# Kernel optimization log

Hardware: AMD Instinct MI355X
Metric: run time of the kernel (lower is better)

The kernel has to match this reference:

```python
import jax, jax.numpy as jnp
import numpy as np

C = 64
K = 3          # kernel_size
EK = 5         # encoder_kernel
PAD = (K - 1) // 2


def _conv(x, w, pad):
    return jax.lax.conv_general_dilated(
        x, w, window_strides=(1, 1), padding=[(pad, pad), (pad, pad)],
        dimension_numbers=('NCHW', 'OIHW', 'NCHW'))


def setup_inputs() -> dict:
    key = jax.random.key(0)
    ks = jax.random.split(key, 6)
    b, h, w = 8, 128, 128
    x = jax.random.normal(ks[0], (b, C, h, w), dtype=jnp.float32)
    # gen_kernel: 1x1 conv (C->C, with bias) then EKxEK conv (C->K*K, no bias)
    w1 = jax.random.normal(ks[1], (C, C, 1, 1), dtype=jnp.float32) * (1.0 / np.sqrt(C))
    b1 = jax.random.normal(ks[2], (C,), dtype=jnp.float32) * 0.01
    w2 = jax.random.normal(ks[3], (K * K, C, EK, EK), dtype=jnp.float32) * (1.0 / np.sqrt(C * EK * EK))
    # consensus t_c: 1x1 conv C->C//4, relu, 1x1 conv C//4->C, relu (no bias)
    tc1 = jax.random.normal(ks[4], (C // 4, C, 1, 1), dtype=jnp.float32) * (1.0 / np.sqrt(C))
    tc2 = jax.random.normal(ks[5], (C, C // 4, 1, 1), dtype=jnp.float32) * (1.0 / np.sqrt(C // 4))
    return {"x": x, "w1": w1, "b1": b1, "w2": w2, "tc1": tc1, "tc2": tc2}


def reference(x, w1, b1, w2, tc1, tc2):
    b, c, h, w = x.shape
    oh, ow = h, w  # stride == 1
    # dynamic kernel logits: (b, K*K, oh, ow)
    y = _conv(x, w1, 0) + b1[None, :, None, None]
    wt = _conv(y, w2, (EK - 1) // 2)
    # consensus scale: adaptive avg pool to 1x1 then mean over batch -> (c,)
    x_con = jnp.mean(x, axis=(0, 2, 3))                      # (c,)
    h1 = jax.nn.relu(jnp.einsum('oc,c->o', tc1[:, :, 0, 0], x_con))
    tmp = jax.nn.relu(jnp.einsum('oc,c->o', tc2[:, :, 0, 0], h1))  # (c,)
    # broadcast logits to (b, c, K*K, oh, ow) and softmax over K*K
    logits = wt[:, None, :, :, :] * tmp[None, :, None, None, None]
    attn = jax.nn.softmax(logits, axis=2)                    # (b,c,9,oh,ow)
    # unfold patches: reflect-pad then 9 shifted views, order kh*K+kw (row-major)
    px = jnp.pad(x, ((0, 0), (0, 0), (PAD, PAD), (PAD, PAD)), mode='reflect')
    pats = jnp.stack([px[:, :, i:i + oh, j:j + ow]
                      for i in range(K) for j in range(K)], axis=2)  # (b,c,9,oh,ow)
    out = jnp.sum(attn * pats, axis=2)                       # (b,c,oh,ow)
    return out
```

## Files before the change

### kernel.cpp

```cpp
#include <hip/hip_runtime.h>
#include <hip/hip_bf16.h>
#include <cstddef>


#define B 8
#define C 64
#define HW 128
#define NK 9
#define NT 25
#define LOG2E 1.4426950408889634f
#define PSTR 72

typedef __attribute__((ext_vector_type(8))) short short8;
typedef __attribute__((ext_vector_type(4))) float float4v;
typedef __attribute__((ext_vector_type(4))) unsigned int uint4v;

__device__ __forceinline__ unsigned short f2bf(float f) {
    unsigned int u = __float_as_uint(f);
    unsigned int r = u + 0x7FFF + ((u >> 16) & 1);
    return (unsigned short)(r >> 16);
}
__device__ __forceinline__ float fast_exp2(float x) {
    float r;
    asm("v_exp_f32 %0, %1" : "=v"(r) : "v"(x));
    return r;
}
__device__ __forceinline__ float fast_rcp(float x) {
    float r;
    asm("v_rcp_f32 %0, %1" : "=v"(r) : "v"(x));
    return r;
}

__global__ __launch_bounds__(256) void xcon_kernel(const float* __restrict__ x,
                                                   float* __restrict__ part) {
    const int c = blockIdx.x >> 2, qb = blockIdx.x & 3;
    float s = 0.f;
    for (int bb = 0; bb < 2; ++bb) {
        const int b = qb * 2 + bb;
        const float4* p = (const float4*)(x + ((size_t)(b * C + c)) * (HW * HW));
        for (int idx = threadIdx.x; idx < (HW * HW) / 4; idx += 256) {
            float4 v = p[idx];
            s += (v.x + v.y) + (v.z + v.w);
        }
    }
    __shared__ float red[256];
    red[threadIdx.x] = s;
    __syncthreads();
    for (int off = 128; off > 0; off >>= 1) {
        if (threadIdx.x < off) red[threadIdx.x] += red[threadIdx.x + off];
        __syncthreads();
    }
    if (threadIdx.x == 0) part[c * 4 + qb] = red[0];
}

__global__ __launch_bounds__(256) void prep_kernel(const float* __restrict__ w1,
                                                   const float* __restrict__ b1,
                                                   const float* __restrict__ w2,
                                                   unsigned short* __restrict__ Abuf,
                                                   float* __restrict__ betaG) {
    if (blockIdx.x < 50) {
        __shared__ float sw2[NK * 64];
        __shared__ float sw1[64 * 32];
        const int chunk = blockIdx.x;
        const int t = chunk >> 1, ch = chunk & 1;
        for (int idx = threadIdx.x; idx < NK * 64; idx += 256) {
            const int m = idx >> 6, cc = idx & 63;
            sw2[idx] = w2[(m * 64 + cc) * NT + t];
        }
        for (int idx = threadIdx.x; idx < 2048; idx += 256) {
            const int cc = idx >> 5, j = idx & 31;
            sw1[idx] = w1[cc * 64 + ch * 32 + j];
        }
        __syncthreads();
        for (int sidx = 0; sidx < 2; ++sidx) {
            const int slot = sidx * 256 + threadIdx.x;
            const int quad = slot >> 7, m = (slot >> 3) & 15, jj = slot & 7;
            unsigned short hi = 0, lo = 0;
            if (m < NK) {
                float s = 0.f;
                for (int cc = 0; cc < 64; ++cc)
                    s += sw2[m * 64 + cc] * sw1[cc * 32 + quad * 8 + jj];
                hi = f2bf(s);
                lo = f2bf(s - __uint_as_float(((unsigned int)hi) << 16));
            }
            Abuf[chunk * 1024 + slot] = hi;
            Abuf[chunk * 1024 + 512 + slot] = lo;
        }
    } else {
        __shared__ float beta_s[NT * NK];
        const int t0 = threadIdx.x;
        if (t0 < NT * NK) {
            const int t = t0 / NK, k = t0 - t * NK;
            float s = 0.f;
            for (int cc = 0; cc < 64; ++cc)
                s += w2[(k * 64 + cc) * NT + t] * b1[cc];
            beta_s[t0] = s;
        }
        __syncthreads();
        if (t0 < 225) {
            const int ic = t0 / 45, jc = (t0 / 9) % 5, k = t0 % 9;
            float s = 0.f;
            for (int eh = 0; eh < 5; ++eh) {
                bool rok = (ic == 0) ? (eh >= 2) : (ic == 1) ? (eh >= 1)
                          : (ic == 3) ? (eh <= 3) : (ic == 4) ? (eh <= 2) : true;
                if (!rok) continue;
                for (int ew = 0; ew < 5; ++ew) {
                    bool cok = (jc == 0) ? (ew >= 2) : (jc == 1) ? (ew >= 1)
                              : (jc == 3) ? (ew <= 3) : (jc == 4) ? (ew <= 2) : true;
                    if (cok) s += beta_s[(eh * 5 + ew) * NK + k];
                }
            }
            betaG[t0] = s;
        }
    }
}

__global__ __launch_bounds__(512, 4) void fused_kernel(const float* __restrict__ x,
                                                       const unsigned short* __restrict__ Abuf,
                                                       const float* __restrict__ betaG,
                                                       const float* __restrict__ part,
                                                       const float* __restrict__ tc1,
                                                       const float* __restrict__ tc2,
                                                       float* __restrict__ out) {
    __shared__ unsigned short stag[400 * PSTR];
    __shared__ float wpart[128 * 10];
    __shared__ float lt[C];
    const int b = blockIdx.y;
    const int i0 = (blockIdx.x >> 3) * 16, j0 = (blockIdx.x & 7) * 16;
    const int tid = threadIdx.x, lane = tid & 63, wid = tid >> 6;
    const int n = lane & 15, q = lane >> 4;
    const int rowg = wid >> 1, h = wid & 1;

    for (int idx = tid; idx < 12800; idx += 512) {
        const int ch = idx / 200;
        const int rem = idx - ch * 200;
        const int li = rem / 10, cp = rem - li * 10;
        const int gi = i0 + li - 2;
        const int gj = j0 + cp * 2 - 2;
        unsigned int pack = 0u;
        if (gi >= 0 && gi < HW && gj >= 0 && gj <= HW - 2) {
            const float2 v = *(const float2*)(x + (((size_t)(b * C + ch)) * HW + gi) * HW + gj);
            pack = (unsigned int)f2bf(v.x) | ((unsigned int)f2bf(v.y) << 16);
        }
        const int p0 = (li * 20 + cp * 2) * PSTR + ch;
        stag[p0] = (unsigned short)(pack & 0xffffu);
        stag[p0 + PSTR] = (unsigned short)(pack >> 16);
    }

    if (wid == 0) {
        float xcv = (part[lane * 4 + 0] + part[lane * 4 + 1]
                   + part[lane * 4 + 2] + part[lane * 4 + 3]) * (1.f / (B * HW * HW));
        float hh = 0.f;
        for (int c = 0; c < C; ++c) {
            float xcc = __shfl(xcv, c);
            if (lane < 16) hh += tc1[lane * C + c] * xcc;
        }
        hh = fmaxf(hh, 0.f);
        float ltv = 0.f;
#pragma unroll
        for (int o = 0; o < 16; ++o) {
            float ho = __shfl(hh, o);
            ltv += tc2[lane * 16 + o] * ho;
        }
        lt[lane] = fmaxf(ltv, 0.f) * LOG2E;
    }

    const int prow = rowg * 4 + q;
    const int pgi = i0 + prow, pgj = j0 + n;
    float bgv[NK];
    if (h == 0) {
        const int ic = pgi < 2 ? pgi : (pgi > 125 ? pgi - 123 : 2);
        const int jc = pgj < 2 ? pgj : (pgj > 125 ? pgj - 123 : 2);
        const float* bp = betaG + (ic * 5 + jc) * NK;
#pragma unroll
        for (int k = 0; k < NK; ++k) bgv[k] = bp[k];
    }

    __syncthreads();

    float4v acc[4];
    const float4v zero4 = {0.f, 0.f, 0.f, 0.f};
#pragma unroll
    for (int g = 0; g < 4; ++g) acc[g] = zero4;

    const unsigned short* Ab = Abuf + h * 1024 + lane * 8;
    const unsigned short* sb = stag + h * 32 + q * 8;
#pragma unroll
    for (int ew = 0; ew < 5; ++ew) {
        short8 w8[8];
#pragma unroll
        for (int rr = 0; rr < 8; ++rr)
            w8[rr] = *(const short8*)(sb + ((rowg * 4 + rr) * 20 + ew + n) * PSTR);
#pragma unroll
        for (int eh = 0; eh < 5; ++eh) {
            const int t = eh * 5 + ew;
            const short8 ahi = *(const short8*)(Ab + t * 2048);
            const short8 alo = *(const short8*)(Ab + t * 2048 + 512);
#pragma unroll
            for (int g = 0; g < 4; ++g) {
                acc[g] = __builtin_amdgcn_mfma_f32_16x16x32_bf16(ahi, w8[g + eh], acc[g], 0, 0, 0);
                acc[g] = __builtin_amdgcn_mfma_f32_16x16x32_bf16(alo, w8[g + eh], acc[g], 0, 0, 0);
            }
        }
    }

    float wv[NK];
#pragma unroll
    for (int k = 0; k < NK; ++k) {
        const int src = (k >> 2) * 16 + n;
        const int rr = k & 3;
        float v0 = __shfl(acc[0][rr], src);
        float v1 = __shfl(acc[1][rr], src);
        float v2 = __shfl(acc[2][rr], src);
        float v3 = __shfl(acc[3][rr], src);
        wv[k] = (q == 0) ? v0 : (q == 1) ? v1 : (q == 2) ? v2 : v3;
    }

    const int lp = ((rowg & 1) << 6) + lane;
    for (int pg = 0; pg < 2; ++pg) {
        const bool inpass = (rowg >> 1) == pg;
        if (pg) __syncthreads();
        if (inpass && h == 1) {
#pragma unroll
            for (int k = 0; k < NK; ++k) wpart[lp * 10 + k] = wv[k];
        }
        __syncthreads();
        if (inpass && h == 0) {
            float w9[NK];
            float wmax = -1e30f;
#pragma unroll
            for (int k = 0; k < NK; ++k) {
                w9[k] = wv[k] + wpart[lp * 10 + k] + bgv[k];
                wmax = fmaxf(wmax, w9[k]);
            }
#pragma unroll
            for (int k = 0; k < NK; ++k) wpart[lp * 10 + k] = w9[k] - wmax;
        }
        __syncthreads();
#pragma unroll
        for (int s = 0; s < 2; ++s) {
            const int task = tid * 2 + s;
            const int lpx = task >> 3, oct = task & 7;
            const int l6 = lpx & 63;
            const int brow = (2 * pg + (lpx >> 6)) * 4 + (l6 >> 4);
            const int bcol = l6 & 15;
            const int bgi = i0 + brow, bgj = j0 + bcol;
            float dv[NK];
#pragma unroll
            for (int k = 0; k < NK; ++k) dv[k] = wpart[lpx * 10 + k];
            int r0 = bgi - 1; r0 = r0 < 0 ? 1 : r0;
            int r2 = bgi + 1; r2 = r2 > 127 ? 126 : r2;
            int c0 = bgj - 1; c0 = c0 < 0 ? 1 : c0;
            int c2 = bgj + 1; c2 = c2 > 127 ? 126 : c2;
            const int R[3] = {r0 - i0 + 2, bgi - i0 + 2, r2 - i0 + 2};
            const int Cc[3] = {c0 - j0 + 2, bgj - j0 + 2, c2 - j0 + 2};
            const unsigned short* sb2 = stag + oct * 8;
            uint4v xs[NK];
#pragma unroll
            for (int kh = 0; kh < 3; ++kh)
#pragma unroll
                for (int kw = 0; kw < 3; ++kw)
                    xs[kh * 3 + kw] = *(const uint4v*)(sb2 + (R[kh] * 20 + Cc[kw]) * PSTR);
            float* outp = out + (((size_t)b * C + oct * 8) * HW + bgi) * HW + bgj;
#pragma unroll
            for (int jj = 0; jj < 4; ++jj) {
                const float t0 = lt[oct * 8 + jj * 2];
                const float t1 = lt[oct * 8 + jj * 2 + 1];
                float s0 = 0.f, o0 = 0.f, s1 = 0.f, o1 = 0.f;
#pragma unroll
                for (int k = 0; k < NK; ++k) {
                    const unsigned int u = xs[k][jj];
                    const float e0 = fast_exp2(dv[k] * t0);
                    const float e1 = fast_exp2(dv[k] * t1);
                    s0 += e0; o0 = fmaf(e0, __uint_as_float(u << 16), o0);
                    s1 += e1; o1 = fmaf(e1, __uint_as_float(u & 0xffff0000u), o1);
                }
                outp[(size_t)(jj * 2) * (HW * HW)] = o0 * fast_rcp(s0);
                outp[(size_t)(jj * 2 + 1) * (HW * HW)] = o1 * fast_rcp(s1);
            }
        }
    }
}

extern "C" void kernel_launch(void* const* d_in, const int* in_sizes, int n_in,
                              void* d_out, int out_size, void* d_ws, size_t ws_size,
                              hipStream_t stream) {
    const float* x   = (const float*)d_in[0];
    const float* w1  = (const float*)d_in[1];
    const float* b1  = (const float*)d_in[2];
    const float* w2  = (const float*)d_in[3];
    const float* tc1 = (const float*)d_in[4];
    const float* tc2 = (const float*)d_in[5];
    float* out = (float*)d_out;

    char* ws = (char*)d_ws;
    float* part  = (float*)(ws + 0);
    unsigned short* Abuf = (unsigned short*)(ws + 1024);
    float* betaG = (float*)(ws + 103424);

    xcon_kernel<<<256, 256, 0, stream>>>(x, part);
    prep_kernel<<<51, 256, 0, stream>>>(w1, b1, w2, Abuf, betaG);
    fused_kernel<<<dim3(64, B), 512, 0, stream>>>(x, Abuf, betaG, part, tc1, tc2, out);
}
```

Measured before the change: 147.6 us.

## Pre-pack x to padded bf16 channel-last layout and stage tiles via global_load_lds

Adds a separate kernel that converts x once into a zero-padded bf16 NHWC-like buffer whose 64-channel vectors are XOR-swizzled. The fused kernel then fills its shared-memory halo tile with direct 16-byte global-to-LDS loads instead of per-element fp32 loads, conversion and scattered 2-byte LDS stores. LDS reads use the matching XOR swizzle in place of the padded stride, to avoid bank conflicts. The trade-off is an extra kernel launch plus a full write and re-read of a bf16 copy of x through global memory.

New measurement: 146.6 us. No clear change (-0.7%).

```diff
diff --git a/kernel.cpp b/kernel.cpp
--- a/kernel.cpp
+++ b/kernel.cpp
@@ -8,8 +8,8 @@
 #define HW 128
 #define NK 9
 #define NT 25
+#define XR 132
 #define LOG2E 1.4426950408889634f
-#define PSTR 72
 
 typedef __attribute__((ext_vector_type(8))) short short8;
 typedef __attribute__((ext_vector_type(4))) float float4v;
@@ -29,6 +29,12 @@
     float r;
     asm("v_rcp_f32 %0, %1" : "=v"(r) : "v"(x));
     return r;
+}
+__device__ __forceinline__ void load_lds16(const unsigned short* g, unsigned short* l) {
+    __builtin_amdgcn_global_load_lds(
+        (const __attribute__((address_space(1))) unsigned int*)g,
+        (__attribute__((address_space(3))) unsigned int*)l,
+        16, 0, 0);
 }
 
 __global__ __launch_bounds__(256) void xcon_kernel(const float* __restrict__ x,
@@ -51,6 +57,43 @@
         __syncthreads();
     }
     if (threadIdx.x == 0) part[c * 4 + qb] = red[0];
+}
+
+__global__ __launch_bounds__(256) void xpack_kernel(const float* __restrict__ x,
+                                                    unsigned short* __restrict__ xbf) {
+    const int r = blockIdx.x, b = blockIdx.y;
+    unsigned short* rowp = xbf + ((size_t)(b * XR + r)) * (XR * 64);
+    const int t = threadIdx.x;
+    if (r < 2 || r >= 130) {
+        const uint4v z = {0u, 0u, 0u, 0u};
+        for (int idx = t; idx < 1056; idx += 256)
+            *(uint4v*)(rowp + idx * 8) = z;
+        return;
+    }
+    const int h = r - 2;
+    if (t < 32) {
+        const uint4v z = {0u, 0u, 0u, 0u};
+        const int q4 = t & 3;
+        const int wc = (q4 < 2) ? q4 : (q4 + 128);
+        *(uint4v*)(rowp + wc * 64 + ((t >> 2) << 3)) = z;
+    }
+    const int c8 = t >> 5;
+    const int wl = t & 31;
+    const float* xp = x + (((size_t)(b * C + c8 * 8)) * HW + h) * HW;
+#pragma unroll
+    for (int k = 0; k < 4; ++k) {
+        const int gw = wl + 32 * k;
+        const int wc = gw + 2;
+        uint4v dv;
+#pragma unroll
+        for (int j = 0; j < 4; ++j) {
+            const float v0 = xp[(size_t)(2 * j) * (HW * HW) + gw];
+            const float v1 = xp[(size_t)(2 * j + 1) * (HW * HW) + gw];
+            dv[j] = (unsigned int)f2bf(v0) | ((unsigned int)f2bf(v1) << 16);
+        }
+        const int sw = ((r & 1) * 4 + wc) & 7;
+        *(uint4v*)(rowp + wc * 64 + ((c8 ^ sw) << 3)) = dv;
+    }
 }
 
 __global__ __launch_bounds__(256) void prep_kernel(const float* __restrict__ w1,
@@ -115,14 +158,14 @@
     }
 }
 
-__global__ __launch_bounds__(512, 4) void fused_kernel(const float* __restrict__ x,
+__global__ __launch_bounds__(512, 4) void fused_kernel(const unsigned short* __restrict__ xbf,
                                                        const unsigned short* __restrict__ Abuf,
                                                        const float* __restrict__ betaG,
                                                        const float* __restrict__ part,
                                                        const float* __restrict__ tc1,
                                                        const float* __restrict__ tc2,
                                                        float* __restrict__ out) {
-    __shared__ unsigned short stag[400 * PSTR];
+    __shared__ __align__(16) unsigned short stag[400 * 64];
     __shared__ float wpart[128 * 10];
     __shared__ float lt[C];
     const int b = blockIdx.y;
@@ -131,20 +174,21 @@
     const int n = lane & 15, q = lane >> 4;
     const int rowg = wid >> 1, h = wid & 1;
 
-    for (int idx = tid; idx < 12800; idx += 512) {
-        const int ch = idx / 200;
-        const int rem = idx - ch * 200;
-        const int li = rem / 10, cp = rem - li * 10;
-        const int gi = i0 + li - 2;
-        const int gj = j0 + cp * 2 - 2;
-        unsigned int pack = 0u;
-        if (gi >= 0 && gi < HW && gj >= 0 && gj <= HW - 2) {
-            const float2 v = *(const float2*)(x + (((size_t)(b * C + ch)) * HW + gi) * HW + gj);
-            pack = (unsigned int)f2bf(v.x) | ((unsigned int)f2bf(v.y) << 16);
-        }
-        const int p0 = (li * 20 + cp * 2) * PSTR + ch;
-        stag[p0] = (unsigned short)(pack & 0xffffu);
-        stag[p0 + PSTR] = (unsigned short)(pack >> 16);
+    {
+        const unsigned short* xrow0 = xbf + (((size_t)(b * XR + i0)) * XR + j0) * 64;
+#pragma unroll
+        for (int k = 0; k < 6; ++k) {
+            const int ci = k * 512 + tid;
+            const int li = ((ci >> 5) * 205) >> 10;
+            const int rem = ci - li * 160;
+            load_lds16(xrow0 + li * (XR * 64) + rem * 8, stag + ci * 8);
+        }
+        if (tid < 128) {
+            const int ci = 3072 + tid;
+            const int li = ((ci >> 5) * 205) >> 10;
+            const int rem = ci - li * 160;
+            load_lds16(xrow0 + li * (XR * 64) + rem * 8, stag + ci * 8);
+        }
     }
 
     if (wid == 0) {
@@ -184,13 +228,16 @@
     for (int g = 0; g < 4; ++g) acc[g] = zero4;
 
     const unsigned short* Ab = Abuf + h * 1024 + lane * 8;
-    const unsigned short* sb = stag + h * 32 + q * 8;
+    const int chs = (h << 2) | q;
+    const int rb = rowg * 4;
 #pragma unroll
     for (int ew = 0; ew < 5; ++ew) {
         short8 w8[8];
 #pragma unroll
-        for (int rr = 0; rr < 8; ++rr)
-            w8[rr] = *(const short8*)(sb + ((rowg * 4 + rr) * 20 + ew + n) * PSTR);
+        for (int rr = 0; rr < 8; ++rr) {
+            const int px = (rb + rr) * 20 + ew + n;
+            w8[rr] = *(const short8*)(stag + px * 64 + ((chs ^ (px & 7)) << 3));
+        }
 #pragma unroll
         for (int eh = 0; eh < 5; ++eh) {
             const int t = eh * 5 + ew;
@@ -254,13 +301,14 @@
             int c2 = bgj + 1; c2 = c2 > 127 ? 126 : c2;
             const int R[3] = {r0 - i0 + 2, bgi - i0 + 2, r2 - i0 + 2};
             const int Cc[3] = {c0 - j0 + 2, bgj - j0 + 2, c2 - j0 + 2};
-            const unsigned short* sb2 = stag + oct * 8;
             uint4v xs[NK];
 #pragma unroll
             for (int kh = 0; kh < 3; ++kh)
 #pragma unroll
-                for (int kw = 0; kw < 3; ++kw)
-                    xs[kh * 3 + kw] = *(const uint4v*)(sb2 + (R[kh] * 20 + Cc[kw]) * PSTR);
+                for (int kw = 0; kw < 3; ++kw) {
+                    const int prc = R[kh] * 20 + Cc[kw];
+                    xs[kh * 3 + kw] = *(const uint4v*)(stag + prc * 64 + ((oct ^ (prc & 7)) << 3));
+                }
             float* outp = out + (((size_t)b * C + oct * 8) * HW + bgi) * HW + bgj;
 #pragma unroll
             for (int jj = 0; jj < 4; ++jj) {
@@ -297,8 +345,10 @@
     float* part  = (float*)(ws + 0);
     unsigned short* Abuf = (unsigned short*)(ws + 1024);
     float* betaG = (float*)(ws + 103424);
+    unsigned short* xbf  = (unsigned short*)(ws + 104448);
 
     xcon_kernel<<<256, 256, 0, stream>>>(x, part);
+    xpack_kernel<<<dim3(XR, B), 256, 0, stream>>>(x, xbf);
     prep_kernel<<<51, 256, 0, stream>>>(w1, b1, w2, Abuf, betaG);
-    fused_kernel<<<dim3(64, B), 512, 0, stream>>>(x, Abuf, betaG, part, tc1, tc2, out);
-}
+    fused_kernel<<<dim3(64, B), 512, 0, stream>>>(xbf, Abuf, betaG, part, tc1, tc2, out);
+}
```
